# Kernel tuning notes

Hardware: AMD Instinct MI355X
Metric: run time of the kernel (lower is better)

The kernel has to match this reference:

```python
import jax, jax.numpy as jnp
import numpy as np

N_SRC, N_DST, E, T, C = 10000, 10000, 320000, 4, 64


def setup_inputs() -> dict:
    key = jax.random.key(0)
    ks = jax.random.split(key, 8)
    return {
        "feat_src": jax.random.normal(ks[0], (N_SRC, T, C), dtype=jnp.float32),
        "feat_dst": jax.random.normal(ks[1], (N_DST, T, C), dtype=jnp.float32),
        "edge_weight": jax.random.uniform(ks[2], (E,), dtype=jnp.float32),
        "weight_e": jax.random.normal(ks[3], (1, C), dtype=jnp.float32) * (6.0 / (1 + C)) ** 0.5,
        "u": jax.random.normal(ks[4], (C, C), dtype=jnp.float32) * (3.0 / C) ** 0.5,
        "v": jax.random.normal(ks[5], (C, C), dtype=jnp.float32) * (3.0 / C) ** 0.5,
        "ln_gamma": jnp.ones((C,), dtype=jnp.float32),
        "ln_beta": jnp.zeros((C,), dtype=jnp.float32),
        "src_idx": jax.random.randint(ks[6], (E,), 0, N_SRC, dtype=jnp.int32),
        "dst_idx": jax.random.randint(ks[7], (E,), 0, N_DST, dtype=jnp.int32),
    }


def reference(feat_src, feat_dst, edge_weight, weight_e, u, v, ln_gamma, ln_beta, src_idx, dst_idx):
    n_dst = feat_dst.shape[0]
    # edge feature projection: [E] -> [E,1] @ [1,C] -> [E,C]
    ew = edge_weight[:, None] @ weight_e
    # node projections: [N,T,C] @ [C,C]
    h_src = jnp.einsum('ntc,cd->ntd', feat_src, u)
    h_dst = jnp.einsum('ntc,cd->ntd', feat_dst, v)
    # per-edge gather
    hs = h_src[src_idx]              # [E,T,C]
    hd = h_dst[dst_idx]              # [E,T,C]
    gate = jax.nn.sigmoid(hs * hd * ew[:, None, :])  # [E,T,C]
    msg = hs * gate                  # [E,T,C]
    # scatter-sum over destination nodes
    aggr = jax.ops.segment_sum(msg, dst_idx, num_segments=n_dst)  # [N_dst,T,C]
    out = jnp.einsum('ntc,cd->ntd', feat_dst, u) + aggr
    # LayerNorm over last dim (normalize == 'ln')
    mean = out.mean(axis=-1, keepdims=True)
    var = out.var(axis=-1, keepdims=True)
    out = (out - mean) * jax.lax.rsqrt(var + 1e-5) * ln_gamma + ln_beta
    return out + feat_dst
```

## Files before the change

kernel.cpp:

```cpp
#include <hip/hip_runtime.h>
#include <math.h>


#define BUCKET 80

typedef short short8 __attribute__((ext_vector_type(8)));
typedef float f32x4  __attribute__((ext_vector_type(4)));

__device__ __forceinline__ unsigned short f2bf(float f) {
    unsigned u = __float_as_uint(f);
    return (unsigned short)((u + 0x7fffu + ((u >> 16) & 1u)) >> 16);
}

__global__ __launch_bounds__(256) void init_kernel(
    int* __restrict__ counts, int n_dst, int2* __restrict__ es, int es_total,
    ushort4* __restrict__ h_srcT, int n_src,
    const float* __restrict__ U, const float* __restrict__ V,
    short8* __restrict__ wfrag) {
    int i = blockIdx.x * 256 + threadIdx.x;
    if (i < n_dst) counts[i] = 0;
    if (i < 64) h_srcT[(size_t)n_src * 64 + i] = make_ushort4(0, 0, 0, 0);
    if (i < es_total) es[i] = make_int2(n_src << 6, 0);
    if (i < 1024) {
        int l = i & 63, ct = (i >> 6) & 3, kc = (i >> 8) & 1, mat = (i >> 9) & 1;
        const float* W = mat ? V : U;
        int col = ct * 16 + (l & 15);
        int k0  = kc * 32 + (l >> 4) * 8;
        short8 s;
#pragma unroll
        for (int j = 0; j < 8; ++j)
            s[j] = (short)f2bf(W[(size_t)(k0 + j) * 64 + col]);
        wfrag[i] = s;
    }
}

__global__ __launch_bounds__(256) void proj_kernel(
    const float* __restrict__ feat_src, const float* __restrict__ feat_dst,
    const float* __restrict__ weight_e,
    const int* __restrict__ src_idx, const int* __restrict__ dst_idx,
    const float* __restrict__ ew, int E,
    const short8* __restrict__ wfrag,
    ushort4* __restrict__ h_srcT, float* __restrict__ h_base, float* __restrict__ h_dst_w,
    int* __restrict__ counts, int2* __restrict__ es,
    int n_src, int n_dst, int nsb) {
    int t = threadIdx.x, b = blockIdx.x;

    for (int e = b * 256 + t; e < E; e += gridDim.x * 256) {
        int d = dst_idx[e];
        int pos = atomicAdd(&counts[d], 1);
        if (pos < BUCKET)
            es[d * BUCKET + pos] = make_int2(src_idx[e] << 6, __float_as_int(ew[e]));
    }

    int type = (b < nsb) ? 0 : (b < 2 * nsb) ? 1 : 2;
    int rb = b - type * nsb;
    int nrows = (type == 0 ? n_src : n_dst) * 4;
    const float* A = (type == 0) ? feat_src : feat_dst;

    int w = t >> 6, l = t & 63;
    int lr = l & 15, lg = l >> 4;

    const short8* wf = wfrag + (type == 2 ? 512 : 0);
    short8 bf[2][4];
#pragma unroll
    for (int kc = 0; kc < 2; ++kc)
#pragma unroll
        for (int ct = 0; ct < 4; ++ct)
            bf[kc][ct] = wf[(kc * 4 + ct) * 64 + l];

#pragma unroll
    for (int e2 = 0; e2 < 2; ++e2) {
        int rs = rb * 128 + w * 32 + e2 * 16;
        int rr = rs + lr; if (rr >= nrows) rr = nrows - 1;

        short8 af[2];
#pragma unroll
        for (int kc = 0; kc < 2; ++kc) {
            const float* ap = A + (size_t)rr * 64 + kc * 32 + lg * 8;
            float4 a0 = *(const float4*)ap;
            float4 a1 = *(const float4*)(ap + 4);
            short8 s;
            s[0] = (short)f2bf(a0.x); s[1] = (short)f2bf(a0.y);
            s[2] = (short)f2bf(a0.z); s[3] = (short)f2bf(a0.w);
            s[4] = (short)f2bf(a1.x); s[5] = (short)f2bf(a1.y);
            s[6] = (short)f2bf(a1.z); s[7] = (short)f2bf(a1.w);
            af[kc] = s;
        }

        f32x4 acc[4];
#pragma unroll
        for (int ct = 0; ct < 4; ++ct) { acc[ct][0]=0.f; acc[ct][1]=0.f; acc[ct][2]=0.f; acc[ct][3]=0.f; }
#pragma unroll
        for (int ct = 0; ct < 4; ++ct) {
            acc[ct] = __builtin_amdgcn_mfma_f32_16x16x32_bf16(af[0], bf[0][ct], acc[ct], 0, 0, 0);
            acc[ct] = __builtin_amdgcn_mfma_f32_16x16x32_bf16(af[1], bf[1][ct], acc[ct], 0, 0, 0);
        }

        if (type == 0) {
            int node = (rs >> 2) + lg;
            if (node < n_src) {
#pragma unroll
                for (int ct = 0; ct < 4; ++ct) {
                    ushort4 st;
                    st.x = f2bf(acc[ct][0]); st.y = f2bf(acc[ct][1]);
                    st.z = f2bf(acc[ct][2]); st.w = f2bf(acc[ct][3]);
                    h_srcT[(size_t)node * 64 + ct * 16 + lr] = st;
                }
            }
        } else if (type == 1) {
#pragma unroll
            for (int ct = 0; ct < 4; ++ct)
#pragma unroll
                for (int q = 0; q < 4; ++q) {
                    int r = rs + lg * 4 + q;
                    if (r < nrows) h_base[(size_t)r * 64 + ct * 16 + lr] = acc[ct][q];
                }
        } else {
            const float nl2e = -1.44269504f;
#pragma unroll
            for (int ct = 0; ct < 4; ++ct) {
                float wm = weight_e[ct * 16 + lr] * nl2e;
#pragma unroll
                for (int q = 0; q < 4; ++q) {
                    int r = rs + lg * 4 + q;
                    if (r < nrows) h_dst_w[(size_t)r * 64 + ct * 16 + lr] = acc[ct][q] * wm;
                }
            }
        }
    }
}

__global__ __launch_bounds__(256) void aggregate_kernel(
    const ushort4* __restrict__ h_srcT,
    const float* __restrict__ h_dst_w, const float* __restrict__ h_base,
    const float* __restrict__ feat_dst,
    const int* __restrict__ counts, const int2* __restrict__ es,
    const float* __restrict__ gamma, const float* __restrict__ beta,
    float* __restrict__ out) {
    __shared__ float xbuf[4][4][64];
    int tid = threadIdx.x;
    int w = tid >> 6, c = tid & 63;
    int d = blockIdx.x;
    size_t rb = (size_t)d * 256;

    float hw0 = h_dst_w[rb +   0 + c];
    float hw1 = h_dst_w[rb +  64 + c];
    float hw2 = h_dst_w[rb + 128 + c];
    float hw3 = h_dst_w[rb + 192 + c];

    int ngroups = (counts[d] + 3) >> 2;
    if (ngroups > BUCKET / 4) ngroups = BUCKET / 4;
    const int2* ep = es + (size_t)d * BUCKET;

    float acc0 = 0.f, acc1 = 0.f, acc2 = 0.f, acc3 = 0.f;

    ushort4 hA[4]; float wA[4];
    int g = w;
#pragma unroll
    for (int i = 0; i < 4; ++i) {
        int2 ev = ep[4 * g + i];
        wA[i] = __int_as_float(ev.y);
        hA[i] = h_srcT[ev.x + c];
    }
    while (g < ngroups) {
        int gn = g + 4;
        ushort4 hB[4]; float wB[4];
#pragma unroll
        for (int i = 0; i < 4; ++i) {
            int2 ev = ep[4 * gn + i];
            wB[i] = __int_as_float(ev.y);
            hB[i] = h_srcT[ev.x + c];
        }
#pragma unroll
        for (int i = 0; i < 4; ++i) {
            float ww = wA[i];
            float hs0 = __uint_as_float((unsigned)hA[i].x << 16);
            float hs1 = __uint_as_float((unsigned)hA[i].y << 16);
            float hs2 = __uint_as_float((unsigned)hA[i].z << 16);
            float hs3 = __uint_as_float((unsigned)hA[i].w << 16);
            float y0 = fminf(hs0 * (hw0 * ww), 30.f);
            float y1 = fminf(hs1 * (hw1 * ww), 30.f);
            float y2 = fminf(hs2 * (hw2 * ww), 30.f);
            float y3 = fminf(hs3 * (hw3 * ww), 30.f);
            float a0 = 1.f + __builtin_amdgcn_exp2f(y0);
            float a1 = 1.f + __builtin_amdgcn_exp2f(y1);
            float a2 = 1.f + __builtin_amdgcn_exp2f(y2);
            float a3 = 1.f + __builtin_amdgcn_exp2f(y3);
            float p01 = a0 * a1, p23 = a2 * a3;
            float R = __builtin_amdgcn_rcpf(p01 * p23);
            float q01 = R * p23, q23 = R * p01;
            acc0 = fmaf(hs0, a1 * q01, acc0);
            acc1 = fmaf(hs1, a0 * q01, acc1);
            acc2 = fmaf(hs2, a3 * q23, acc2);
            acc3 = fmaf(hs3, a2 * q23, acc3);
        }
#pragma unroll
        for (int i = 0; i < 4; ++i) { hA[i] = hB[i]; wA[i] = wB[i]; }
        g = gn;
    }

    xbuf[w][0][c] = acc0;
    xbuf[w][1][c] = acc1;
    xbuf[w][2][c] = acc2;
    xbuf[w][3][c] = acc3;
    __syncthreads();
    float f = xbuf[0][w][c] + xbuf[1][w][c] + xbuf[2][w][c] + xbuf[3][w][c]
            + h_base[rb + w * 64 + c];

    float s1 = f, s2 = f * f;
#pragma unroll
    for (int off = 32; off >= 1; off >>= 1) {
        s1 += __shfl_xor(s1, off, 64);
        s2 += __shfl_xor(s2, off, 64);
    }
    const float inv64 = 1.f / 64.f;
    float mean = s1 * inv64;
    float var  = s2 * inv64 - mean * mean;
    float inv  = rsqrtf(var + 1e-5f);
    out[rb + w * 64 + c] = (f - mean) * inv * gamma[c] + beta[c] + feat_dst[rb + w * 64 + c];
}

extern "C" void kernel_launch(void* const* d_in, const int* in_sizes, int n_in,
                              void* d_out, int out_size, void* d_ws, size_t ws_size,
                              hipStream_t stream) {
    const float* feat_src    = (const float*)d_in[0];
    const float* feat_dst    = (const float*)d_in[1];
    const float* edge_weight = (const float*)d_in[2];
    const float* weight_e    = (const float*)d_in[3];
    const float* u           = (const float*)d_in[4];
    const float* v           = (const float*)d_in[5];
    const float* ln_gamma    = (const float*)d_in[6];
    const float* ln_beta     = (const float*)d_in[7];
    const int*   src_idx     = (const int*)d_in[8];
    const int*   dst_idx     = (const int*)d_in[9];
    float* out = (float*)d_out;

    int E     = in_sizes[2];
    int n_src = in_sizes[0] / 256;
    int n_dst = in_sizes[1] / 256;

    int es_total = n_dst * BUCKET + 64;

    ushort4* h_srcT  = (ushort4*)d_ws;
    float* h_base    = (float*)(h_srcT + (size_t)(n_src + 1) * 64);
    float* h_dst_w   = h_base + (size_t)n_dst * 256;
    int2*  es        = (int2*)(h_dst_w + (size_t)n_dst * 256);
    short8* wfrag    = (short8*)(es + es_total);
    int*   counts    = (int*)(wfrag + 1024);

    int nsb = (n_src * 4 + 127) / 128;

    init_kernel<<<(es_total + 255) / 256, 256, 0, stream>>>(counts, n_dst, es, es_total,
                                                            h_srcT, n_src, u, v, wfrag);
    proj_kernel<<<3 * nsb, 256, 0, stream>>>(feat_src, feat_dst, weight_e,
                                             src_idx, dst_idx, edge_weight, E,
                                             wfrag, h_srcT, h_base, h_dst_w,
                                             counts, es, n_src, n_dst, nsb);
    aggregate_kernel<<<n_dst, 256, 0, stream>>>(h_srcT, h_dst_w, h_base,
                                                feat_dst, counts, es,
                                                ln_gamma, ln_beta, out);
}
```

Measured before the change: 74.32 us.

## Use nontemporal loads/stores for streaming buffers and simplify sigmoid gate math

Marks streaming reads and writes (edge indices, features, intermediate projections, bucket entries, output) as nontemporal so they do not pollute cache, leaving more cache room for the randomly gathered h_src rows. The sigmoid gate also changes from the shared-reciprocal trick to one rcp per element and drops the clamp. Nontemporal stores on data that is read again in the next kernel (es, h_base, h_dst_w) may lose cache hits that previously helped, and the unclamped exp2 can overflow to inf, where rcp gives 0, which is still the correct limit.

```diff
diff --git a/kernel.cpp b/kernel.cpp
--- a/kernel.cpp
+++ b/kernel.cpp
@@ -6,6 +6,8 @@
 
 typedef short short8 __attribute__((ext_vector_type(8)));
 typedef float f32x4  __attribute__((ext_vector_type(4)));
+typedef float f32x4e __attribute__((ext_vector_type(4)));
+typedef int   int2e  __attribute__((ext_vector_type(2)));
 
 __device__ __forceinline__ unsigned short f2bf(float f) {
     unsigned u = __float_as_uint(f);
@@ -13,14 +15,17 @@
 }
 
 __global__ __launch_bounds__(256) void init_kernel(
-    int* __restrict__ counts, int n_dst, int2* __restrict__ es, int es_total,
+    int* __restrict__ counts, int n_dst, int2e* __restrict__ es, int es_total,
     ushort4* __restrict__ h_srcT, int n_src,
     const float* __restrict__ U, const float* __restrict__ V,
     short8* __restrict__ wfrag) {
     int i = blockIdx.x * 256 + threadIdx.x;
     if (i < n_dst) counts[i] = 0;
     if (i < 64) h_srcT[(size_t)n_src * 64 + i] = make_ushort4(0, 0, 0, 0);
-    if (i < es_total) es[i] = make_int2(n_src << 6, 0);
+    if (i < es_total) {
+        int2e s; s[0] = n_src << 6; s[1] = 0;
+        __builtin_nontemporal_store(s, es + i);
+    }
     if (i < 1024) {
         int l = i & 63, ct = (i >> 6) & 3, kc = (i >> 8) & 1, mat = (i >> 9) & 1;
         const float* W = mat ? V : U;
@@ -41,15 +46,19 @@
     const float* __restrict__ ew, int E,
     const short8* __restrict__ wfrag,
     ushort4* __restrict__ h_srcT, float* __restrict__ h_base, float* __restrict__ h_dst_w,
-    int* __restrict__ counts, int2* __restrict__ es,
+    int* __restrict__ counts, int2e* __restrict__ es,
     int n_src, int n_dst, int nsb) {
     int t = threadIdx.x, b = blockIdx.x;
 
     for (int e = b * 256 + t; e < E; e += gridDim.x * 256) {
-        int d = dst_idx[e];
+        int d = __builtin_nontemporal_load(dst_idx + e);
+        int s = __builtin_nontemporal_load(src_idx + e);
+        float w = __builtin_nontemporal_load(ew + e);
         int pos = atomicAdd(&counts[d], 1);
-        if (pos < BUCKET)
-            es[d * BUCKET + pos] = make_int2(src_idx[e] << 6, __float_as_int(ew[e]));
+        if (pos < BUCKET) {
+            int2e v; v[0] = s << 6; v[1] = __float_as_int(w);
+            __builtin_nontemporal_store(v, es + (size_t)d * BUCKET + pos);
+        }
     }
 
     int type = (b < nsb) ? 0 : (b < 2 * nsb) ? 1 : 2;
@@ -77,13 +86,13 @@
 #pragma unroll
         for (int kc = 0; kc < 2; ++kc) {
             const float* ap = A + (size_t)rr * 64 + kc * 32 + lg * 8;
-            float4 a0 = *(const float4*)ap;
-            float4 a1 = *(const float4*)(ap + 4);
+            f32x4e a0 = __builtin_nontemporal_load((const f32x4e*)ap);
+            f32x4e a1 = __builtin_nontemporal_load((const f32x4e*)(ap + 4));
             short8 s;
-            s[0] = (short)f2bf(a0.x); s[1] = (short)f2bf(a0.y);
-            s[2] = (short)f2bf(a0.z); s[3] = (short)f2bf(a0.w);
-            s[4] = (short)f2bf(a1.x); s[5] = (short)f2bf(a1.y);
-            s[6] = (short)f2bf(a1.z); s[7] = (short)f2bf(a1.w);
+            s[0] = (short)f2bf(a0[0]); s[1] = (short)f2bf(a0[1]);
+            s[2] = (short)f2bf(a0[2]); s[3] = (short)f2bf(a0[3]);
+            s[4] = (short)f2bf(a1[0]); s[5] = (short)f2bf(a1[1]);
+            s[6] = (short)f2bf(a1[2]); s[7] = (short)f2bf(a1[3]);
             af[kc] = s;
         }
 
@@ -113,7 +122,9 @@
 #pragma unroll
                 for (int q = 0; q < 4; ++q) {
                     int r = rs + lg * 4 + q;
-                    if (r < nrows) h_base[(size_t)r * 64 + ct * 16 + lr] = acc[ct][q];
+                    if (r < nrows)
+                        __builtin_nontemporal_store(acc[ct][q],
+                            h_base + (size_t)r * 64 + ct * 16 + lr);
                 }
         } else {
             const float nl2e = -1.44269504f;
@@ -123,7 +134,9 @@
 #pragma unroll
                 for (int q = 0; q < 4; ++q) {
                     int r = rs + lg * 4 + q;
-                    if (r < nrows) h_dst_w[(size_t)r * 64 + ct * 16 + lr] = acc[ct][q] * wm;
+                    if (r < nrows)
+                        __builtin_nontemporal_store(acc[ct][q] * wm,
+                            h_dst_w + (size_t)r * 64 + ct * 16 + lr);
                 }
             }
         }
@@ -134,7 +147,7 @@
     const ushort4* __restrict__ h_srcT,
     const float* __restrict__ h_dst_w, const float* __restrict__ h_base,
     const float* __restrict__ feat_dst,
-    const int* __restrict__ counts, const int2* __restrict__ es,
+    const int* __restrict__ counts, const int2e* __restrict__ es,
     const float* __restrict__ gamma, const float* __restrict__ beta,
     float* __restrict__ out) {
     __shared__ float xbuf[4][4][64];
@@ -143,14 +156,14 @@
     int d = blockIdx.x;
     size_t rb = (size_t)d * 256;
 
-    float hw0 = h_dst_w[rb +   0 + c];
-    float hw1 = h_dst_w[rb +  64 + c];
-    float hw2 = h_dst_w[rb + 128 + c];
-    float hw3 = h_dst_w[rb + 192 + c];
+    float hw0 = __builtin_nontemporal_load(h_dst_w + rb +   0 + c);
+    float hw1 = __builtin_nontemporal_load(h_dst_w + rb +  64 + c);
+    float hw2 = __builtin_nontemporal_load(h_dst_w + rb + 128 + c);
+    float hw3 = __builtin_nontemporal_load(h_dst_w + rb + 192 + c);
 
     int ngroups = (counts[d] + 3) >> 2;
     if (ngroups > BUCKET / 4) ngroups = BUCKET / 4;
-    const int2* ep = es + (size_t)d * BUCKET;
+    const int2e* ep = es + (size_t)d * BUCKET;
 
     float acc0 = 0.f, acc1 = 0.f, acc2 = 0.f, acc3 = 0.f;
 
@@ -158,18 +171,18 @@
     int g = w;
 #pragma unroll
     for (int i = 0; i < 4; ++i) {
-        int2 ev = ep[4 * g + i];
-        wA[i] = __int_as_float(ev.y);
-        hA[i] = h_srcT[ev.x + c];
+        int2e ev = __builtin_nontemporal_load(ep + 4 * g + i);
+        wA[i] = __int_as_float(ev[1]);
+        hA[i] = h_srcT[ev[0] + c];
     }
     while (g < ngroups) {
         int gn = g + 4;
         ushort4 hB[4]; float wB[4];
 #pragma unroll
         for (int i = 0; i < 4; ++i) {
-            int2 ev = ep[4 * gn + i];
-            wB[i] = __int_as_float(ev.y);
-            hB[i] = h_srcT[ev.x + c];
+            int2e ev = __builtin_nontemporal_load(ep + 4 * gn + i);
+            wB[i] = __int_as_float(ev[1]);
+            hB[i] = h_srcT[ev[0] + c];
         }
 #pragma unroll
         for (int i = 0; i < 4; ++i) {
@@ -178,21 +191,14 @@
             float hs1 = __uint_as_float((unsigned)hA[i].y << 16);
             float hs2 = __uint_as_float((unsigned)hA[i].z << 16);
             float hs3 = __uint_as_float((unsigned)hA[i].w << 16);
-            float y0 = fminf(hs0 * (hw0 * ww), 30.f);
-            float y1 = fminf(hs1 * (hw1 * ww), 30.f);
-            float y2 = fminf(hs2 * (hw2 * ww), 30.f);
-            float y3 = fminf(hs3 * (hw3 * ww), 30.f);
-            float a0 = 1.f + __builtin_amdgcn_exp2f(y0);
-            float a1 = 1.f + __builtin_amdgcn_exp2f(y1);
-            float a2 = 1.f + __builtin_amdgcn_exp2f(y2);
-            float a3 = 1.f + __builtin_amdgcn_exp2f(y3);
-            float p01 = a0 * a1, p23 = a2 * a3;
-            float R = __builtin_amdgcn_rcpf(p01 * p23);
-            float q01 = R * p23, q23 = R * p01;
-            acc0 = fmaf(hs0, a1 * q01, acc0);
-            acc1 = fmaf(hs1, a0 * q01, acc1);
-            acc2 = fmaf(hs2, a3 * q23, acc2);
-            acc3 = fmaf(hs3, a2 * q23, acc3);
+            float g0 = __builtin_amdgcn_rcpf(1.f + __builtin_amdgcn_exp2f(hs0 * (hw0 * ww)));
+            float g1 = __builtin_amdgcn_rcpf(1.f + __builtin_amdgcn_exp2f(hs1 * (hw1 * ww)));
+            float g2 = __builtin_amdgcn_rcpf(1.f + __builtin_amdgcn_exp2f(hs2 * (hw2 * ww)));
+            float g3 = __builtin_amdgcn_rcpf(1.f + __builtin_amdgcn_exp2f(hs3 * (hw3 * ww)));
+            acc0 = fmaf(hs0, g0, acc0);
+            acc1 = fmaf(hs1, g1, acc1);
+            acc2 = fmaf(hs2, g2, acc2);
+            acc3 = fmaf(hs3, g3, acc3);
         }
 #pragma unroll
         for (int i = 0; i < 4; ++i) { hA[i] = hB[i]; wA[i] = wB[i]; }
@@ -205,7 +211,7 @@
     xbuf[w][3][c] = acc3;
     __syncthreads();
     float f = xbuf[0][w][c] + xbuf[1][w][c] + xbuf[2][w][c] + xbuf[3][w][c]
-            + h_base[rb + w * 64 + c];
+            + __builtin_nontemporal_load(h_base + rb + w * 64 + c);
 
     float s1 = f, s2 = f * f;
 #pragma unroll
@@ -217,7 +223,9 @@
     float mean = s1 * inv64;
     float var  = s2 * inv64 - mean * mean;
     float inv  = rsqrtf(var + 1e-5f);
-    out[rb + w * 64 + c] = (f - mean) * inv * gamma[c] + beta[c] + feat_dst[rb + w * 64 + c];
+    float r = (f - mean) * inv * gamma[c] + beta[c]
+            + __builtin_nontemporal_load(feat_dst + rb + w * 64 + c);
+    __builtin_nontemporal_store(r, out + rb + w * 64 + c);
 }
 
 extern "C" void kernel_launch(void* const* d_in, const int* in_sizes, int n_in,
@@ -244,7 +252,7 @@
     ushort4* h_srcT  = (ushort4*)d_ws;
     float* h_base    = (float*)(h_srcT + (size_t)(n_src + 1) * 64);
     float* h_dst_w   = h_base + (size_t)n_dst * 256;
-    int2*  es        = (int2*)(h_dst_w + (size_t)n_dst * 256);
+    int2e* es        = (int2e*)(h_dst_w + (size_t)n_dst * 256);
     short8* wfrag    = (short8*)(es + es_total);
     int*   counts    = (int*)(wfrag + 1024);
 
```

Result: slower. 83.98 us (+13.0%).
